# Optimization experiments

Measured on AMD Instinct MI355X. Metric: run time of the kernel, lower is better.

## Reference

```python
import jax, jax.numpy as jnp
import numpy as np

N, IN, H, D, OUT = 2048, 256, 12, 32, 384
ALPHA = 0.2


def setup_inputs() -> dict:
    key = jax.random.key(0)
    ks = jax.random.split(key, 12)
    s = 0.05
    return {
        "x": jax.random.normal(ks[0], (N, IN), jnp.float32),
        "adj": jax.random.uniform(ks[1], (N, N), jnp.float32),  # all > 0 -> fully connected mask
        "W": jax.random.normal(ks[2], (H * D, IN), jnp.float32) * s,
        "attn_src": jax.random.normal(ks[3], (H, D), jnp.float32) * s,
        "attn_dst": jax.random.normal(ks[4], (H, D), jnp.float32) * s,
        "edge_W": jax.random.normal(ks[5], (H, 1), jnp.float32) * s,
        "edge_b": jax.random.normal(ks[6], (H,), jnp.float32) * s,
        "res_W": jax.random.normal(ks[7], (H * D, IN), jnp.float32) * s,
        "res_b": jax.random.normal(ks[8], (H * D,), jnp.float32) * s,
        "fus_W": jax.random.normal(ks[9], (OUT, H * D), jnp.float32) * s,
        "fus_b": jax.random.normal(ks[10], (OUT,), jnp.float32) * s,
    }


def reference(x, adj, W, attn_src, attn_dst, edge_W, edge_b, res_W, res_b, fus_W, fus_b):
    n = x.shape[0]
    h = (x @ W.T).reshape(n, H, D)                      # [N,H,D]
    a_src = jnp.einsum("nhd,hd->nh", h, attn_src)       # [N,H]
    a_dst = jnp.einsum("nhd,hd->nh", h, attn_dst)       # [N,H]
    attn = a_src[:, None, :] + a_dst[None, :, :]        # [N,N,H]
    # edge_encoder: Linear(1 -> H) applied to adj[...,None]
    attn = attn + adj[..., None] * edge_W.reshape(1, 1, H) + edge_b
    mask = (adj > 0)[..., None]                         # [N,N,1]
    attn = jnp.where(mask, attn, -jnp.inf)
    attn = jnp.where(attn >= 0, attn, ALPHA * attn)     # leaky_relu
    attn = jax.nn.softmax(attn, axis=1)                 # over source nodes j
    # dropout is identity in eval mode
    h_out = jnp.einsum("ijh,jhd->ihd", attn, h).reshape(n, H * D)
    h_out = h_out + x @ res_W.T + res_b                 # residual
    out = jax.nn.gelu(h_out @ fus_W.T + fus_b, approximate=False)
    return out
```

## Files before the change

kernel.cpp:

```cpp
#include <hip/hip_runtime.h>
#include <hip/hip_bf16.h>

#define NN 2048
#define NH 12
#define HD 32
#define CALL 384

typedef float f32x16 __attribute__((ext_vector_type(16)));
typedef _Float16 f16x4 __attribute__((ext_vector_type(4)));

static __device__ __forceinline__ f32x16 mfma8f16(f16x4 a, f16x4 b, f32x16 c) {
    return __builtin_amdgcn_mfma_f32_32x32x8f16(a, b, c, 0, 0, 0);
}
static __device__ __forceinline__ f16x4 u2f(uint2 u) {
    union { uint2 u2; f16x4 f; } c; c.u2 = u; return c.f;
}

__global__ __launch_bounds__(256) void gemm01(
    const float* __restrict__ A, const float* __restrict__ B0,
    const float* __restrict__ B1, const float* __restrict__ bias1,
    const float* __restrict__ attn_src, const float* __restrict__ attn_dst,
    _Float16* __restrict__ outT, float* __restrict__ outF,
    float* __restrict__ asrc, float* __restrict__ adstT)
{
    __shared__ _Float16 As[64][36];
    __shared__ _Float16 Bs[64][36];
    const int t = threadIdx.x;
    const int w = t >> 6, l = t & 63, g = l >> 5, il = l & 31;
    const int m0 = blockIdx.x * 64, n0 = blockIdx.y * 64;
    const int mode = blockIdx.z;
    const float* B = mode ? B1 : B0;
    const int wr = (w >> 1) * 32, wc = (w & 1) * 32;
    const int ti = t >> 2, seg = t & 3;
    const int Kdim = 256;

    f32x16 acc;
#pragma unroll
    for (int r = 0; r < 16; ++r) acc[r] = 0.f;

    for (int kk = 0; kk < Kdim; kk += 32) {
        __syncthreads();
        {
            const float* Ap = A + (size_t)(m0 + ti) * Kdim + kk + seg * 8;
            float4 v0 = *reinterpret_cast<const float4*>(Ap);
            float4 v1 = *reinterpret_cast<const float4*>(Ap + 4);
            f16x4 lo = {(_Float16)v0.x, (_Float16)v0.y, (_Float16)v0.z, (_Float16)v0.w};
            f16x4 hi = {(_Float16)v1.x, (_Float16)v1.y, (_Float16)v1.z, (_Float16)v1.w};
            *reinterpret_cast<f16x4*>(&As[ti][seg * 8])     = lo;
            *reinterpret_cast<f16x4*>(&As[ti][seg * 8 + 4]) = hi;
        }
        {
            const float* Bp = B + (size_t)(n0 + ti) * Kdim + kk + seg * 8;
            float4 v0 = *reinterpret_cast<const float4*>(Bp);
            float4 v1 = *reinterpret_cast<const float4*>(Bp + 4);
            f16x4 lo = {(_Float16)v0.x, (_Float16)v0.y, (_Float16)v0.z, (_Float16)v0.w};
            f16x4 hi = {(_Float16)v1.x, (_Float16)v1.y, (_Float16)v1.z, (_Float16)v1.w};
            *reinterpret_cast<f16x4*>(&Bs[ti][seg * 8])     = lo;
            *reinterpret_cast<f16x4*>(&Bs[ti][seg * 8 + 4]) = hi;
        }
        __syncthreads();
#pragma unroll
        for (int kc = 0; kc < 4; ++kc) {
            f16x4 af = *reinterpret_cast<const f16x4*>(&As[wr + il][kc * 8 + 4 * g]);
            f16x4 bf = *reinterpret_cast<const f16x4*>(&Bs[wc + il][kc * 8 + 4 * g]);
            acc = mfma8f16(af, bf, acc);
        }
    }

    const int colg = n0 + wc + il;
    if (mode == 0) {
#pragma unroll
        for (int q = 0; q < 4; ++q) {
            const int row = m0 + wr + 8 * q + 4 * g;
            f16x4 v;
#pragma unroll
            for (int r = 0; r < 4; ++r) v[r] = (_Float16)acc[4 * q + r];
            *reinterpret_cast<f16x4*>(&outT[(size_t)colg * NN + row]) = v;
        }
        const int hstar = colg >> 5;
        const float sv = attn_src[hstar * HD + il];
        const float dv = attn_dst[hstar * HD + il];
        float ps[16], pd[16];
#pragma unroll
        for (int r = 0; r < 16; ++r) { ps[r] = acc[r] * sv; pd[r] = acc[r] * dv; }
#pragma unroll
        for (int m = 1; m <= 16; m <<= 1) {
#pragma unroll
            for (int r = 0; r < 16; ++r) {
                ps[r] += __shfl_xor(ps[r], m);
                pd[r] += __shfl_xor(pd[r], m);
            }
        }
        if (il == 0) {
#pragma unroll
            for (int r = 0; r < 16; ++r) {
                const int row = m0 + wr + (r & 3) + 8 * (r >> 2) + 4 * g;
                asrc[row * NH + hstar] = ps[r];
                adstT[(size_t)hstar * NN + row] = pd[r] * 1.44269504089f;
            }
        }
    } else {
        const float bs = bias1[colg];
#pragma unroll
        for (int reg = 0; reg < 16; ++reg) {
            const int row = m0 + wr + (reg & 3) + 8 * (reg >> 2) + 4 * g;
            outF[(size_t)row * CALL + colg] = acc[reg] + bs;
        }
    }
}

__global__ __launch_bounds__(256) void gemm2(
    const _Float16* __restrict__ A16, const float* __restrict__ B,
    const float* __restrict__ bias, float* __restrict__ outF)
{
    __shared__ _Float16 As[64][36];
    __shared__ _Float16 Bs[64][36];
    const int t = threadIdx.x;
    const int w = t >> 6, l = t & 63, g = l >> 5, il = l & 31;
    const int m0 = blockIdx.x * 64, n0 = blockIdx.y * 64;
    const int wr = (w >> 1) * 32, wc = (w & 1) * 32;
    const int ti = t >> 2, seg = t & 3;
    const int Kdim = 384;

    f32x16 acc;
#pragma unroll
    for (int r = 0; r < 16; ++r) acc[r] = 0.f;

    for (int kk = 0; kk < Kdim; kk += 32) {
        __syncthreads();
        {
            const uint4 v = *reinterpret_cast<const uint4*>(A16 + (size_t)(m0 + ti) * Kdim + kk + seg * 8);
            *reinterpret_cast<uint2*>(&As[ti][seg * 8])     = make_uint2(v.x, v.y);
            *reinterpret_cast<uint2*>(&As[ti][seg * 8 + 4]) = make_uint2(v.z, v.w);
        }
        {
            const float* Bp = B + (size_t)(n0 + ti) * Kdim + kk + seg * 8;
            float4 v0 = *reinterpret_cast<const float4*>(Bp);
            float4 v1 = *reinterpret_cast<const float4*>(Bp + 4);
            f16x4 lo = {(_Float16)v0.x, (_Float16)v0.y, (_Float16)v0.z, (_Float16)v0.w};
            f16x4 hi = {(_Float16)v1.x, (_Float16)v1.y, (_Float16)v1.z, (_Float16)v1.w};
            *reinterpret_cast<f16x4*>(&Bs[ti][seg * 8])     = lo;
            *reinterpret_cast<f16x4*>(&Bs[ti][seg * 8 + 4]) = hi;
        }
        __syncthreads();
#pragma unroll
        for (int kc = 0; kc < 4; ++kc) {
            f16x4 af = *reinterpret_cast<const f16x4*>(&As[wr + il][kc * 8 + 4 * g]);
            f16x4 bf = *reinterpret_cast<const f16x4*>(&Bs[wc + il][kc * 8 + 4 * g]);
            acc = mfma8f16(af, bf, acc);
        }
    }

    const int colg = n0 + wc + il;
    const float bs = bias[colg];
#pragma unroll
    for (int reg = 0; reg < 16; ++reg) {
        const int row = m0 + wr + (reg & 3) + 8 * (reg >> 2) + 4 * g;
        float vv = acc[reg] + bs;
        vv = 0.5f * vv * (1.0f + erff(vv * 0.70710678118f));
        outF[(size_t)row * CALL + colg] = vv;
    }
}

__global__ __launch_bounds__(1024, 4) void attn6(
    const float* __restrict__ adj, const _Float16* __restrict__ hT,
    const float* __restrict__ asrc, const float* __restrict__ adstT,
    const float* __restrict__ eW, const float* __restrict__ eb,
    const float* __restrict__ res, _Float16* __restrict__ hsum)
{
    __shared__ __align__(16) char smem[55296];
    const int t = threadIdx.x;
    const int w = t >> 6, l = t & 63, g = l >> 5, il = l & 31;
    const int band = blockIdx.x & 63, hg = blockIdx.x >> 6;
    const int i0 = band * 32, h0 = hg * 3, c0 = hg * 96;

    float* adst_s = (float*)(smem + w * 1536);
    float* red    = (float*)smem;
    float* dsum_s = (float*)(smem + 49152);

    const float LOG2E = 1.44269504089f;
    float base_h[3], eWr[3];
#pragma unroll
    for (int hh = 0; hh < 3; ++hh) {
        base_h[hh] = (asrc[(size_t)(i0 + il) * NH + h0 + hh] + eb[h0 + hh]) * LOG2E;
        eWr[hh] = eW[h0 + hh] * LOG2E;
    }

    const int jbase = w * 128;
#pragma unroll
    for (int p = 0; p < 6; ++p) {
        const int idx = p * 64 + l;
        adst_s[idx] = adstT[(size_t)(h0 + (idx >> 7)) * NN + jbase + (idx & 127)];
    }

    f32x16 acc[3];
#pragma unroll
    for (int hh = 0; hh < 3; ++hh)
#pragma unroll
        for (int r = 0; r < 16; ++r) acc[hh][r] = 0.f;
    float dsum[3] = {0.f, 0.f, 0.f};

    const _Float16* hbase = hT  + (size_t)(c0 + il) * NN + jbase + 16 * g;
    const float*    abase = adj + (size_t)(i0 + il) * NN + jbase + 16 * g;

    float4 ajc[4], ajn[4];
#pragma unroll
    for (int p = 0; p < 4; ++p)
        ajc[p] = *reinterpret_cast<const float4*>(abase + 4 * p);

#pragma unroll 1
    for (int tl = 0; tl < 4; ++tl) {
        const int jo = tl * 32;
        if (tl < 3) {
#pragma unroll
            for (int p = 0; p < 4; ++p)
                ajn[p] = *reinterpret_cast<const float4*>(abase + jo + 32 + 4 * p);
        }
#pragma unroll
        for (int hh = 0; hh < 3; ++hh) {
            const _Float16* hp = hbase + (size_t)(hh * 32) * NN + jo;
            const uint4 hA = *reinterpret_cast<const uint4*>(hp);
            const uint4 hB = *reinterpret_cast<const uint4*>(hp + 8);
#pragma unroll
            for (int ks = 0; ks < 4; ++ks) {
                const float4 a4 = ajc[ks];
                const float4 ad = *reinterpret_cast<const float4*>(
                    &adst_s[hh * 128 + jo + 16 * g + 4 * ks]);
                f16x4 ef;
#pragma unroll
                for (int jj = 0; jj < 4; ++jj) {
                    const float ajv = (&a4.x)[jj];
                    float tt = fmaf(ajv, eWr[hh], base_h[hh] + (&ad.x)[jj]);
                    tt = fmaxf(tt, 0.2f * tt);
                    const float ee = ajv > 0.f ? exp2f(tt) : 0.f;
                    dsum[hh] += ee;
                    ef[jj] = (_Float16)ee;
                }
                const uint2 hu = (ks == 0) ? make_uint2(hA.x, hA.y)
                               : (ks == 1) ? make_uint2(hA.z, hA.w)
                               : (ks == 2) ? make_uint2(hB.x, hB.y)
                                           : make_uint2(hB.z, hB.w);
                acc[hh] = mfma8f16(ef, u2f(hu), acc[hh]);
            }
        }
#pragma unroll
        for (int p = 0; p < 4; ++p) ajc[p] = ajn[p];
    }

    __syncthreads();
#pragma unroll
    for (int hh = 0; hh < 3; ++hh) {
        const float dtot = dsum[hh] + __shfl_xor(dsum[hh], 32);
        if (g == 0) dsum_s[(w * 3 + hh) * 32 + il] = dtot;
    }
    if (w < 4) {
#pragma unroll
        for (int hh = 0; hh < 3; ++hh)
#pragma unroll
            for (int reg = 0; reg < 16; ++reg)
                red[((w * 3 + hh) * 16 + reg) * 64 + l] = acc[hh][reg];
    }
    __syncthreads();
    if (w >= 4 && w < 8) {
#pragma unroll
        for (int hh = 0; hh < 3; ++hh)
#pragma unroll
            for (int reg = 0; reg < 16; ++reg)
                red[(((w - 4) * 3 + hh) * 16 + reg) * 64 + l] += acc[hh][reg];
    }
    __syncthreads();
    if (w >= 8 && w < 12) {
#pragma unroll
        for (int hh = 0; hh < 3; ++hh)
#pragma unroll
            for (int reg = 0; reg < 16; ++reg)
                red[(((w - 8) * 3 + hh) * 16 + reg) * 64 + l] += acc[hh][reg];
    }
    __syncthreads();
    if (w >= 12) {
#pragma unroll
        for (int hh = 0; hh < 3; ++hh)
#pragma unroll
            for (int reg = 0; reg < 16; ++reg)
                red[(((w - 12) * 3 + hh) * 16 + reg) * 64 + l] += acc[hh][reg];
    }
    __syncthreads();

    {
        const int reg = w;
        const int row_off = (reg & 3) + 8 * (reg >> 2) + 4 * g;
        const int row = i0 + row_off;
#pragma unroll
        for (int hh = 0; hh < 3; ++hh) {
            float v = 0.f, d = 0.f;
#pragma unroll
            for (int q = 0; q < 4; ++q)
                v += red[((q * 3 + hh) * 16 + reg) * 64 + l];
#pragma unroll
            for (int ww = 0; ww < 16; ++ww)
                d += dsum_s[(ww * 3 + hh) * 32 + row_off];
            const int col = (h0 + hh) * 32 + il;
            hsum[(size_t)row * CALL + col] = (_Float16)(v / d + res[(size_t)row * CALL + col]);
        }
    }
}

extern "C" void kernel_launch(void* const* d_in, const int* in_sizes, int n_in,
                              void* d_out, int out_size, void* d_ws, size_t ws_size,
                              hipStream_t stream)
{
    const float* x        = (const float*)d_in[0];
    const float* adj      = (const float*)d_in[1];
    const float* W        = (const float*)d_in[2];
    const float* attn_src = (const float*)d_in[3];
    const float* attn_dst = (const float*)d_in[4];
    const float* edge_W   = (const float*)d_in[5];
    const float* edge_b   = (const float*)d_in[6];
    const float* res_W    = (const float*)d_in[7];
    const float* res_b    = (const float*)d_in[8];
    const float* fus_W    = (const float*)d_in[9];
    const float* fus_b    = (const float*)d_in[10];
    float* out = (float*)d_out;

    char* ws = (char*)d_ws;
    size_t off = 0;
    auto alloc = [&](size_t bytes) { void* p = ws + off; off = (off + bytes + 255) & ~(size_t)255; return p; };
    _Float16* hT    = (_Float16*)alloc((size_t)CALL * NN * 2);
    float*    res   = (float*)alloc((size_t)NN * CALL * 4);
    float*    asrc  = (float*)alloc((size_t)NN * NH * 4);
    float*    adstT = (float*)alloc((size_t)NH * NN * 4);
    _Float16* hsum  = (_Float16*)alloc((size_t)NN * CALL * 2);
    (void)ws_size;

    gemm01<<<dim3(32, 6, 2), dim3(256), 0, stream>>>(x, W, res_W, res_b, attn_src, attn_dst, hT, res, asrc, adstT);
    attn6<<<256, dim3(1024), 0, stream>>>(adj, hT, asrc, adstT, edge_W, edge_b, res, hsum);
    gemm2<<<dim3(32, 6), dim3(256), 0, stream>>>(hsum, fus_W, fus_b, out);
}
```

Baseline: 56.16 us.

## Split K across two wave groups in the projection GEMMs with an LDS reduction

Both small GEMM kernels now use 512 threads per block. Each block loads a 64-wide K slab per step instead of 32, halving the number of sync iterations, and two groups of four waves each handle half of the slab. A shared-memory reduction then combines the partial accumulators before the epilogue. This adds waves per block to hide load latency in grids of only 384 and 192 blocks, at the cost of an extra reduction pass and two barriers.

```diff
diff --git a/kernel.cpp b/kernel.cpp
--- a/kernel.cpp
+++ b/kernel.cpp
@@ -16,29 +16,35 @@
     union { uint2 u2; f16x4 f; } c; c.u2 = u; return c.f;
 }
 
-__global__ __launch_bounds__(256) void gemm01(
+__global__ __launch_bounds__(512) void gemm01(
     const float* __restrict__ A, const float* __restrict__ B0,
     const float* __restrict__ B1, const float* __restrict__ bias1,
     const float* __restrict__ attn_src, const float* __restrict__ attn_dst,
     _Float16* __restrict__ outT, float* __restrict__ outF,
     float* __restrict__ asrc, float* __restrict__ adstT)
 {
-    __shared__ _Float16 As[64][36];
-    __shared__ _Float16 Bs[64][36];
+    __shared__ __align__(16) char smem[17408];
+    _Float16 (*As)[68] = (_Float16(*)[68])(smem);
+    _Float16 (*Bs)[68] = (_Float16(*)[68])(smem + 8704);
+    float* red = (float*)smem;
+
     const int t = threadIdx.x;
     const int w = t >> 6, l = t & 63, g = l >> 5, il = l & 31;
+    const int q = w & 3, kg = w >> 2;
     const int m0 = blockIdx.x * 64, n0 = blockIdx.y * 64;
     const int mode = blockIdx.z;
     const float* B = mode ? B1 : B0;
-    const int wr = (w >> 1) * 32, wc = (w & 1) * 32;
-    const int ti = t >> 2, seg = t & 3;
+    const int wr = (q >> 1) * 32, wc = (q & 1) * 32;
+    const int ti = t >> 3, seg = t & 7;
     const int Kdim = 256;
 
     f32x16 acc;
 #pragma unroll
     for (int r = 0; r < 16; ++r) acc[r] = 0.f;
 
-    for (int kk = 0; kk < Kdim; kk += 32) {
+#pragma unroll 1
+    for (int ss = 0; ss < 4; ++ss) {
+        const int kk = ss * 64;
         __syncthreads();
         {
             const float* Ap = A + (size_t)(m0 + ti) * Kdim + kk + seg * 8;
@@ -61,20 +67,30 @@
         __syncthreads();
 #pragma unroll
         for (int kc = 0; kc < 4; ++kc) {
-            f16x4 af = *reinterpret_cast<const f16x4*>(&As[wr + il][kc * 8 + 4 * g]);
-            f16x4 bf = *reinterpret_cast<const f16x4*>(&Bs[wc + il][kc * 8 + 4 * g]);
+            f16x4 af = *reinterpret_cast<const f16x4*>(&As[wr + il][kg * 32 + kc * 8 + 4 * g]);
+            f16x4 bf = *reinterpret_cast<const f16x4*>(&Bs[wc + il][kg * 32 + kc * 8 + 4 * g]);
             acc = mfma8f16(af, bf, acc);
         }
     }
+
+    __syncthreads();
+    if (kg == 1) {
+#pragma unroll
+        for (int r = 0; r < 16; ++r) red[(q * 16 + r) * 64 + l] = acc[r];
+    }
+    __syncthreads();
+    if (kg != 0) return;
+#pragma unroll
+    for (int r = 0; r < 16; ++r) acc[r] += red[(q * 16 + r) * 64 + l];
 
     const int colg = n0 + wc + il;
     if (mode == 0) {
 #pragma unroll
-        for (int q = 0; q < 4; ++q) {
-            const int row = m0 + wr + 8 * q + 4 * g;
+        for (int p = 0; p < 4; ++p) {
+            const int row = m0 + wr + 8 * p + 4 * g;
             f16x4 v;
 #pragma unroll
-            for (int r = 0; r < 4; ++r) v[r] = (_Float16)acc[4 * q + r];
+            for (int r = 0; r < 4; ++r) v[r] = (_Float16)acc[4 * p + r];
             *reinterpret_cast<f16x4*>(&outT[(size_t)colg * NN + row]) = v;
         }
         const int hstar = colg >> 5;
@@ -102,31 +118,37 @@
     } else {
         const float bs = bias1[colg];
 #pragma unroll
-        for (int reg = 0; reg < 16; ++reg) {
-            const int row = m0 + wr + (reg & 3) + 8 * (reg >> 2) + 4 * g;
-            outF[(size_t)row * CALL + colg] = acc[reg] + bs;
-        }
-    }
-}
-
-__global__ __launch_bounds__(256) void gemm2(
+        for (int r = 0; r < 16; ++r) {
+            const int row = m0 + wr + (r & 3) + 8 * (r >> 2) + 4 * g;
+            outF[(size_t)row * CALL + colg] = acc[r] + bs;
+        }
+    }
+}
+
+__global__ __launch_bounds__(512) void gemm2(
     const _Float16* __restrict__ A16, const float* __restrict__ B,
     const float* __restrict__ bias, float* __restrict__ outF)
 {
-    __shared__ _Float16 As[64][36];
-    __shared__ _Float16 Bs[64][36];
+    __shared__ __align__(16) char smem[17408];
+    _Float16 (*As)[68] = (_Float16(*)[68])(smem);
+    _Float16 (*Bs)[68] = (_Float16(*)[68])(smem + 8704);
+    float* red = (float*)smem;
+
     const int t = threadIdx.x;
     const int w = t >> 6, l = t & 63, g = l >> 5, il = l & 31;
+    const int q = w & 3, kg = w >> 2;
     const int m0 = blockIdx.x * 64, n0 = blockIdx.y * 64;
-    const int wr = (w >> 1) * 32, wc = (w & 1) * 32;
-    const int ti = t >> 2, seg = t & 3;
+    const int wr = (q >> 1) * 32, wc = (q & 1) * 32;
+    const int ti = t >> 3, seg = t & 7;
     const int Kdim = 384;
 
     f32x16 acc;
 #pragma unroll
     for (int r = 0; r < 16; ++r) acc[r] = 0.f;
 
-    for (int kk = 0; kk < Kdim; kk += 32) {
+#pragma unroll 1
+    for (int ss = 0; ss < 6; ++ss) {
+        const int kk = ss * 64;
         __syncthreads();
         {
             const uint4 v = *reinterpret_cast<const uint4*>(A16 + (size_t)(m0 + ti) * Kdim + kk + seg * 8);
@@ -145,18 +167,28 @@
         __syncthreads();
 #pragma unroll
         for (int kc = 0; kc < 4; ++kc) {
-            f16x4 af = *reinterpret_cast<const f16x4*>(&As[wr + il][kc * 8 + 4 * g]);
-            f16x4 bf = *reinterpret_cast<const f16x4*>(&Bs[wc + il][kc * 8 + 4 * g]);
+            f16x4 af = *reinterpret_cast<const f16x4*>(&As[wr + il][kg * 32 + kc * 8 + 4 * g]);
+            f16x4 bf = *reinterpret_cast<const f16x4*>(&Bs[wc + il][kg * 32 + kc * 8 + 4 * g]);
             acc = mfma8f16(af, bf, acc);
         }
     }
+
+    __syncthreads();
+    if (kg == 1) {
+#pragma unroll
+        for (int r = 0; r < 16; ++r) red[(q * 16 + r) * 64 + l] = acc[r];
+    }
+    __syncthreads();
+    if (kg != 0) return;
+#pragma unroll
+    for (int r = 0; r < 16; ++r) acc[r] += red[(q * 16 + r) * 64 + l];
 
     const int colg = n0 + wc + il;
     const float bs = bias[colg];
 #pragma unroll
-    for (int reg = 0; reg < 16; ++reg) {
-        const int row = m0 + wr + (reg & 3) + 8 * (reg >> 2) + 4 * g;
-        float vv = acc[reg] + bs;
+    for (int r = 0; r < 16; ++r) {
+        const int row = m0 + wr + (r & 3) + 8 * (r >> 2) + 4 * g;
+        float vv = acc[r] + bs;
         vv = 0.5f * vv * (1.0f + erff(vv * 0.70710678118f));
         outF[(size_t)row * CALL + colg] = vv;
     }
@@ -294,8 +326,8 @@
         for (int hh = 0; hh < 3; ++hh) {
             float v = 0.f, d = 0.f;
 #pragma unroll
-            for (int q = 0; q < 4; ++q)
-                v += red[((q * 3 + hh) * 16 + reg) * 64 + l];
+            for (int p = 0; p < 4; ++p)
+                v += red[((p * 3 + hh) * 16 + reg) * 64 + l];
 #pragma unroll
             for (int ww = 0; ww < 16; ++ww)
                 d += dsum_s[(ww * 3 + hh) * 32 + row_off];
@@ -332,7 +364,7 @@
     _Float16* hsum  = (_Float16*)alloc((size_t)NN * CALL * 2);
     (void)ws_size;
 
-    gemm01<<<dim3(32, 6, 2), dim3(256), 0, stream>>>(x, W, res_W, res_b, attn_src, attn_dst, hT, res, asrc, adstT);
+    gemm01<<<dim3(32, 6, 2), dim3(512), 0, stream>>>(x, W, res_W, res_b, attn_src, attn_dst, hT, res, asrc, adstT);
     attn6<<<256, dim3(1024), 0, stream>>>(adj, hT, asrc, adstT, edge_W, edge_b, res, hsum);
-    gemm2<<<dim3(32, 6), dim3(256), 0, stream>>>(hsum, fus_W, fus_b, out);
-}
+    gemm2<<<dim3(32, 6), dim3(512), 0, stream>>>(hsum, fus_W, fus_b, out);
+}
```

Measured after the change: 52.54 us. 1.07x faster.
